# Optimization experiments

Measured on AMD Instinct MI355X. Metric: run time of the kernel, lower is better.

## Reference

```python
import jax, jax.numpy as jnp
import numpy as np

K = 7
TOWERS = 4
X_SIZE = 8
POS_SIZE = 3
NUM_GRAPHS = 128
NODES_PER_GRAPH = 512
N = NUM_GRAPHS * NODES_PER_GRAPH
EPS_STD = 1e-5  # PyG StdAggregation eps
BN_EPS = 1e-5
# degree histogram passed to PNAConv.__init__ -> avg log-degree used by scalers
_DEG_HIST = np.array([0, 0, 0, 0, 0, 100, 200, 700], dtype=np.float64)
_BINS = np.arange(_DEG_HIST.shape[0], dtype=np.float64)
AVG_DEG_LOG = float((np.log(_BINS + 1.0) * _DEG_HIST).sum() / _DEG_HIST.sum())


def knn_graph(pos, num_graphs, k):
    # batched kNN (loop=False): each node gets its k nearest neighbors within its graph
    Nn, D = pos.shape
    n = Nn // num_graphs
    p = pos.reshape(num_graphs, n, D)
    d2 = jnp.sum((p[:, :, None, :] - p[:, None, :, :]) ** 2, axis=-1)  # [B,n,n]
    d2 = d2 + jnp.eye(n, dtype=d2.dtype) * 1e10  # exclude self-loops
    _, idx = jax.lax.top_k(-d2, k)  # [B,n,k] local neighbor ids
    offs = (jnp.arange(num_graphs) * n)[:, None, None]
    return (idx + offs).reshape(Nn, k)  # global source ids per target node


def pna_conv(x, nbr, W_pre, b_pre, W_post, b_post, W_lin, b_lin):
    # PyG PNAConv, towers=4, pre_layers=1, post_layers=1, divide_input=False, edge_dim=None
    Nn, F = x.shape
    k = nbr.shape[1]
    x_j = x[nbr]                                              # gather sources [N,k,F]
    x_i = jnp.broadcast_to(x[:, None, :], (Nn, k, F))         # target features
    h = jnp.concatenate([x_i, x_j], axis=-1)                  # [N,k,2F]
    m = jnp.einsum('nke,tef->nktf', h, W_pre) + b_pre         # per-tower pre-MLP [N,k,T,F]
    mean = m.mean(axis=1)
    mn = m.min(axis=1)
    mx = m.max(axis=1)
    var = jnp.mean(m * m, axis=1) - mean * mean               # PyG VarAggregation
    std = jnp.sqrt(jax.nn.relu(var) + EPS_STD)
    agg = jnp.concatenate([mean, mn, mx, std], axis=-1)       # [N,T,4F]
    amp = jnp.log(k + 1.0) / AVG_DEG_LOG                      # deg == k for every node in a knn graph
    scaled = jnp.concatenate([agg, agg * amp, agg * (1.0 / amp)], axis=-1)  # identity/amp/atten [N,T,12F]
    out = jnp.concatenate([jnp.broadcast_to(x[:, None, :], (Nn, TOWERS, F)), scaled], axis=-1)  # [N,T,13F]
    out = jnp.einsum('ntg,tgf->ntf', out, W_post) + b_post    # per-tower post-MLP [N,T,F_out]
    out = out.reshape(Nn, -1)
    return out @ W_lin + b_lin                                # mixing Linear(out,out)


def batch_norm(x, g, b):
    # training-mode BatchNorm1d over the node dimension
    mu = x.mean(axis=0)
    var = x.var(axis=0)
    return g * (x - mu) * jax.lax.rsqrt(var + BN_EPS) + b


def forward(x, pos, W_pre1, b_pre1, W_post1, b_post1, W_lin1, b_lin1, bn1_g, bn1_b,
            W_pre2, b_pre2, W_post2, b_post2, W_lin2, b_lin2, bn2_g, bn2_b, num_graphs):
    nbr = knn_graph(pos, num_graphs, K)
    h = jax.nn.relu(batch_norm(pna_conv(x, nbr, W_pre1, b_pre1, W_post1, b_post1, W_lin1, b_lin1), bn1_g, bn1_b))
    h = jax.nn.relu(batch_norm(pna_conv(h, nbr, W_pre2, b_pre2, W_post2, b_post2, W_lin2, b_lin2), bn2_g, bn2_b))
    return h.reshape(num_graphs, -1, h.shape[-1]).mean(axis=1)  # global mean pool -> [B,128]


def _winit(key, shape):
    fan_in = shape[-2]
    return (jax.random.normal(key, shape, dtype=jnp.float32) / jnp.sqrt(jnp.float32(fan_in))).astype(jnp.float32)


def setup_inputs() -> dict:
    key = jax.random.key(0)
    ks = jax.random.split(key, 8)
    F1, F2 = X_SIZE, 64
    return {
        'x': jax.random.normal(ks[0], (N, X_SIZE), dtype=jnp.float32),
        'pos': jax.random.normal(ks[1], (N, POS_SIZE), dtype=jnp.float32),
        'W_pre1': _winit(ks[2], (TOWERS, 2 * F1, F1)),
        'b_pre1': jnp.zeros((TOWERS, F1), jnp.float32),
        'W_post1': _winit(ks[3], (TOWERS, 13 * F1, 64 // TOWERS)),
        'b_post1': jnp.zeros((TOWERS, 64 // TOWERS), jnp.float32),
        'W_lin1': _winit(ks[4], (64, 64)),
        'b_lin1': jnp.zeros((64,), jnp.float32),
        'bn1_g': jnp.ones((64,), jnp.float32),
        'bn1_b': jnp.zeros((64,), jnp.float32),
        'W_pre2': _winit(ks[5], (TOWERS, 2 * F2, F2)),
        'b_pre2': jnp.zeros((TOWERS, F2), jnp.float32),
        'W_post2': _winit(ks[6], (TOWERS, 13 * F2, 128 // TOWERS)),
        'b_post2': jnp.zeros((TOWERS, 128 // TOWERS), jnp.float32),
        'W_lin2': _winit(ks[7], (128, 128)),
        'b_lin2': jnp.zeros((128,), jnp.float32),
        'bn2_g': jnp.ones((128,), jnp.float32),
        'bn2_b': jnp.zeros((128,), jnp.float32),
        'num_graphs': NUM_GRAPHS,
    }


def reference(x, pos, W_pre1, b_pre1, W_post1, b_post1, W_lin1, b_lin1, bn1_g, bn1_b,
              W_pre2, b_pre2, W_post2, b_post2, W_lin2, b_lin2, bn2_g, bn2_b, num_graphs):
    return forward(x, pos, W_pre1, b_pre1, W_post1, b_post1, W_lin1, b_lin1, bn1_g, bn1_b,
                   W_pre2, b_pre2, W_post2, b_post2, W_lin2, b_lin2, bn2_g, bn2_b, num_graphs)
```

## Files before the change

kernel.cpp:

```cpp
#include <hip/hip_runtime.h>
#include <math.h>


#define NGRAPH 128
#define NPG    512
#define NN     (NGRAPH*NPG)
#define KNB    7

constexpr double AVG_DEG_LOG_D = 2.0239670479173344;
constexpr double LOG8_D        = 2.0794415416798357;

typedef _Float16 f16x8 __attribute__((ext_vector_type(8)));
typedef _Float16 h2    __attribute__((ext_vector_type(2)));
typedef float    f32x4 __attribute__((ext_vector_type(4)));

__device__ __forceinline__ unsigned short f2h(float x) {
    _Float16 h = (_Float16)x;
    return __builtin_bit_cast(unsigned short, h);
}

__global__ __launch_bounds__(256) void prep_kernel(
    const float* __restrict__ Wpost1, const float* __restrict__ Wpost2,
    const float* __restrict__ Wpre2,  const float* __restrict__ Wlin2,
    const float* __restrict__ Wlin1,  const float* __restrict__ bpost1,
    const float* __restrict__ blin1,
    const float* __restrict__ bpost2, const float* __restrict__ blin2,
    unsigned short* __restrict__ Wf1p, unsigned short* __restrict__ Wf1l,
    float* __restrict__ blin1_eff,
    unsigned short* __restrict__ Wfuv,
    unsigned short* __restrict__ Wfp, unsigned short* __restrict__ Wfl,
    float* __restrict__ blin_eff)
{
    const float AMP = (float)(LOG8_D / AVG_DEG_LOG_D);
    const float ATT = (float)(AVG_DEG_LOG_D / LOG8_D);
    for (int i = blockIdx.x*256 + threadIdx.x; i < 98496; i += gridDim.x*256) {
        if (i < 4096) {
            int t = i >> 10, kk = (i >> 9) & 1, lane = (i >> 3) & 63, j = i & 7;
            int k = kk*32 + ((lane >> 4) << 3) + j;
            int col = lane & 15;
            float val;
            if (k < 8)       val = Wpost1[(t*104 + k)*16 + col];
            else if (k < 40) {
                int g2 = k - 8;
                val = Wpost1[(t*104 +  8 + g2)*16 + col]
                    + AMP*Wpost1[(t*104 + 40 + g2)*16 + col]
                    + ATT*Wpost1[(t*104 + 72 + g2)*16 + col];
            } else val = 0.f;
            Wf1p[i] = f2h(val);
        } else if (i < 8192) {
            int jj = i - 4096;
            int kk = jj >> 11, tile = (jj >> 9) & 3, lane = (jj >> 3) & 63, j = jj & 7;
            int k = kk*32 + ((lane >> 4) << 3) + j;
            int col = tile*16 + (lane & 15);
            Wf1l[jj] = f2h(Wlin1[k*64 + col]);
        } else if (i < 8256) {
            int c = i - 8192;
            float s = blin1[c];
            for (int o = 0; o < 64; ++o) s += bpost1[o]*Wlin1[o*64 + c];
            blin1_eff[c] = s;
        } else if (i < 41024) {
            int jj = i - 8256;
            int kk = jj >> 14, ct = (jj >> 9) & 31, lane = (jj >> 3) & 63, jf = jj & 7;
            int k   = kk*32 + ((lane >> 4) << 3) + jf;
            int col = ct*16 + (lane & 15);
            float val;
            if (col < 256) { int t = col >> 6, f = col & 63; val = Wpre2[(t*128 +      k)*64 + f]; }
            else { int c2 = col - 256; int t = c2 >> 6, f = c2 & 63; val = Wpre2[(t*128 + 64 + k)*64 + f]; }
            Wfuv[jj] = f2h(val);
        } else if (i < 81984) {
            int jj = i - 41024;
            int t = jj / 10240, r = jj % 10240;
            int kk = r / 1024, r2 = r % 1024;
            int c = r2 >> 9, lane = (r2 >> 3) & 63, jf = r2 & 7;
            int G   = kk*32 + ((lane >> 4) << 3) + jf;
            int col = c*16 + (lane & 15);
            float val;
            if (G < 64) val = Wpost2[(t*832 + G)*32 + col];
            else {
                int g2 = G - 64;
                val = Wpost2[(t*832 +  64 + g2)*32 + col]
                    + AMP*Wpost2[(t*832 + 320 + g2)*32 + col]
                    + ATT*Wpost2[(t*832 + 576 + g2)*32 + col];
            }
            Wfp[jj] = f2h(val);
        } else if (i < 98368) {
            int jj = i - 81984;
            int kk = jj / 4096, r = jj % 4096;
            int tile = r >> 9, lane = (r >> 3) & 63, jf = r & 7;
            int k   = kk*32 + ((lane >> 4) << 3) + jf;
            int col = tile*16 + (lane & 15);
            Wfl[jj] = f2h(Wlin2[k*128 + col]);
        } else {
            int c = i - 98368;
            float s = blin2[c];
            for (int o = 0; o < 128; ++o) s += bpost2[o]*Wlin2[o*128 + c];
            blin_eff[c] = s;
        }
    }
}

__global__ __launch_bounds__(256) void knn_kernel(const float* __restrict__ pos, int* __restrict__ nbr)
{
    __shared__ float4 posS[NPG];
    const int g    = blockIdx.x >> 1;
    const int half = blockIdx.x & 1;
    const int gb   = g * NPG;
    for (int j = threadIdx.x; j < NPG; j += 256)
        posS[j] = make_float4(pos[(gb+j)*3+0], pos[(gb+j)*3+1], pos[(gb+j)*3+2], 0.f);
    __syncthreads();
    const int i = half*256 + threadIdx.x;
    const float4 pi = posS[i];
    float bd[KNB]; int bi[KNB];
#pragma unroll
    for (int e = 0; e < KNB; ++e) { bd[e] = 3.0e38f; bi[e] = -1; }
#pragma unroll 4
    for (int j = 0; j < NPG; ++j) {
        float4 pj = posS[j];
        float dx = pi.x - pj.x, dy = pi.y - pj.y, dz = pi.z - pj.z;
        float d2 = __fadd_rn(__fadd_rn(__fmul_rn(dx,dx), __fmul_rn(dy,dy)), __fmul_rn(dz,dz));
        if (j == i) d2 = __builtin_inff();
        bool cmp[KNB];
#pragma unroll
        for (int e = 0; e < KNB; ++e) cmp[e] = d2 < bd[e];
#pragma unroll
        for (int e = KNB-1; e >= 1; --e) {
            bd[e] = cmp[e-1] ? bd[e-1] : (cmp[e] ? d2 : bd[e]);
            bi[e] = cmp[e-1] ? bi[e-1] : (cmp[e] ? j  : bi[e]);
        }
        bd[0] = cmp[0] ? d2 : bd[0];
        bi[0] = cmp[0] ? j  : bi[0];
    }
#pragma unroll
    for (int e = 0; e < KNB; ++e) nbr[(gb+i)*KNB + e] = gb + bi[e];
}

__global__ __launch_bounds__(256) void a1_kernel(
    const float* __restrict__ x, const float* __restrict__ Wpre1, const float* __restrict__ bpre1,
    float* __restrict__ u1, float* __restrict__ v1)
{
    __shared__ float wS[512];
    __shared__ float bS[32];
    const int tid = threadIdx.x;
    wS[tid] = Wpre1[tid]; wS[tid+256] = Wpre1[tid+256];
    if (tid < 32) bS[tid] = bpre1[tid];
    __syncthreads();
    const int n  = blockIdx.x*8 + (tid>>5);
    const int tf = tid & 31;
    const int t = tf >> 3, f = tf & 7;
    float u = bS[tf], v = 0.f;
#pragma unroll
    for (int e = 0; e < 8; ++e) {
        float xv = x[n*8+e];
        u += xv * wS[(t*16 + e)*8 + f];
        v += xv * wS[(t*16 + 8 + e)*8 + f];
    }
    u1[n*32+tf] = u;
    v1[n*32+tf] = v;
}

__global__ __launch_bounds__(256) void b1_kernel(
    const float* __restrict__ x, const int* __restrict__ nbr,
    const float* __restrict__ u1, const float* __restrict__ v1,
    const unsigned short* __restrict__ Wf1p, const unsigned short* __restrict__ Wf1l,
    const float* __restrict__ blin1_eff,
    float* __restrict__ y1)
{
    __shared__ int nbrsS[112];
    __shared__ __align__(16) unsigned short actS[64*72];
    __shared__ __align__(16) unsigned short postS[16*72];
    const int tid  = threadIdx.x;
    const int base = blockIdx.x * 16;
    if (tid < 112) nbrsS[tid] = nbr[base*7 + tid];
    for (int i = tid; i < 384; i += 256) {
        int r = i / 6, gq = i - 6*r;
        *(ushort4*)&actS[r*72 + 40 + gq*4] = make_ushort4(0,0,0,0);
    }
#pragma unroll
    for (int it = 0; it < 2; ++it) {
        int i = tid + it*256;
        int n = i >> 5, r2 = i & 31, t = r2 >> 3, f = r2 & 7;
        actS[(n*4 + t)*72 + f] = f2h(x[(base+n)*8 + f]);
    }
    __syncthreads();
    {
        const int n = tid >> 4, cp = tid & 15;
        const int tf0 = cp*2, t = tf0 >> 3, f0 = tf0 & 7;
        float2 uu = *(const float2*)&u1[(base+n)*32 + tf0];
        float s0=0.f,s1=0.f,q0=0.f,q1=0.f;
        float mn0=3e38f,mn1=3e38f,mx0=-3e38f,mx1=-3e38f;
#pragma unroll
        for (int e = 0; e < 7; ++e) {
            float2 vv = *(const float2*)&v1[nbrsS[n*7+e]*32 + tf0];
            s0 += vv.x; q0 += vv.x*vv.x; mn0 = fminf(mn0, vv.x); mx0 = fmaxf(mx0, vv.x);
            s1 += vv.y; q1 += vv.y*vv.y; mn1 = fminf(mn1, vv.y); mx1 = fmaxf(mx1, vv.y);
        }
        float me0 = s0*(1.f/7.f), me1 = s1*(1.f/7.f);
        float sd0 = sqrtf(fmaxf(q0*(1.f/7.f) - me0*me0, 0.f) + 1e-5f);
        float sd1 = sqrtf(fmaxf(q1*(1.f/7.f) - me1*me1, 0.f) + 1e-5f);
        const int row = (n*4 + t)*72;
        ushort2 w_;
        w_.x = f2h(uu.x + me0); w_.y = f2h(uu.y + me1); *(ushort2*)&actS[row +  8 + f0] = w_;
        w_.x = f2h(uu.x + mn0); w_.y = f2h(uu.y + mn1); *(ushort2*)&actS[row + 16 + f0] = w_;
        w_.x = f2h(uu.x + mx0); w_.y = f2h(uu.y + mx1); *(ushort2*)&actS[row + 24 + f0] = w_;
        w_.x = f2h(sd0);        w_.y = f2h(sd1);        *(ushort2*)&actS[row + 32 + f0] = w_;
    }
    __syncthreads();
    const int l = tid & 63, w = tid >> 6;
    const int lr = l & 15, lk = l >> 4;
    f32x4 acc = {0.f,0.f,0.f,0.f};
    {
        const f16x8* WB = (const f16x8*)Wf1p;
#pragma unroll
        for (int kk = 0; kk < 2; ++kk) {
            f16x8 a = *(const f16x8*)&actS[(lr*4 + w)*72 + kk*32 + lk*8];
            f16x8 b = WB[(w*2 + kk)*64 + l];
            acc = __builtin_amdgcn_mfma_f32_16x16x32_f16(a, b, acc, 0, 0, 0);
        }
    }
#pragma unroll
    for (int j = 0; j < 4; ++j)
        postS[(lk*4 + j)*72 + w*16 + lr] = f2h(acc[j]);
    __syncthreads();
    f32x4 d = {0.f,0.f,0.f,0.f};
    {
        const f16x8* WB = (const f16x8*)Wf1l;
#pragma unroll
        for (int kk = 0; kk < 2; ++kk) {
            f16x8 a = *(const f16x8*)&postS[lr*72 + kk*32 + lk*8];
            f16x8 b = WB[(kk*4 + w)*64 + l];
            d = __builtin_amdgcn_mfma_f32_16x16x32_f16(a, b, d, 0, 0, 0);
        }
    }
    const float be = blin1_eff[w*16 + lr];
#pragma unroll
    for (int j = 0; j < 4; ++j)
        y1[(base + lk*4 + j)*64 + w*16 + lr] = d[j] + be;
}

template<int C>
__global__ __launch_bounds__(256) void bn_stats_kernel(
    const float* __restrict__ y, float* __restrict__ Ps, float* __restrict__ Pq)
{
    constexpr int IT     = (NN/1024)*(C/4)/256;
    constexpr int GROUPS = C/4;
    constexpr int REPS   = 256/GROUPS;
    const int tid = threadIdx.x;
    const float4* y4 = (const float4*)y + (size_t)blockIdx.x*256*IT;
    float4 s = make_float4(0.f,0.f,0.f,0.f), q = make_float4(0.f,0.f,0.f,0.f);
#pragma unroll
    for (int it = 0; it < IT; ++it) {
        float4 v = y4[it*256 + tid];
        s.x += v.x; s.y += v.y; s.z += v.z; s.w += v.w;
        q.x += v.x*v.x; q.y += v.y*v.y; q.z += v.z*v.z; q.w += v.w*v.w;
    }
    __shared__ float4 sS[256], qS[256];
    sS[tid] = s; qS[tid] = q;
    __syncthreads();
#pragma unroll
    for (int step = REPS/2; step >= 1; step >>= 1) {
        if (tid < step*GROUPS) {
            float4 s2 = sS[tid + step*GROUPS], q2 = qS[tid + step*GROUPS];
            float4 ss = sS[tid], qq = qS[tid];
            ss.x += s2.x; ss.y += s2.y; ss.z += s2.z; ss.w += s2.w;
            qq.x += q2.x; qq.y += q2.y; qq.z += q2.z; qq.w += q2.w;
            sS[tid] = ss; qS[tid] = qq;
        }
        __syncthreads();
    }
    if (tid < GROUPS) {
        ((float4*)&Ps[(size_t)blockIdx.x*C])[tid] = sS[tid];
        ((float4*)&Pq[(size_t)blockIdx.x*C])[tid] = qS[tid];
    }
}

template<int C>
__global__ __launch_bounds__(C) void finA_kernel(
    const float* __restrict__ Ps, const float* __restrict__ Pq,
    float* __restrict__ As, float* __restrict__ Aq)
{
    const int c = threadIdx.x, b = blockIdx.x;
    float s = 0.f, q = 0.f;
#pragma unroll
    for (int i = 0; i < 16; ++i) {
        s += Ps[(b*16 + i)*C + c];
        q += Pq[(b*16 + i)*C + c];
    }
    As[b*C + c] = s;
    Aq[b*C + c] = q;
}

template<int C>
__global__ __launch_bounds__(C) void fin_kernel(
    const float* __restrict__ As, const float* __restrict__ Aq,
    const float* __restrict__ g, const float* __restrict__ b,
    float* __restrict__ scO, float* __restrict__ shO)
{
    const int c = threadIdx.x;
    float s = 0.f, q = 0.f;
#pragma unroll 8
    for (int i = 0; i < 64; ++i) { s += As[i*C + c]; q += Aq[i*C + c]; }
    const float inv = 1.f/(float)NN;
    float mu  = s*inv;
    float var = q*inv - mu*mu;
    float sc  = g[c]*rsqrtf(var + 1e-5f);
    scO[c] = sc;
    shO[c] = b[c] - mu*sc;
}

__global__ __launch_bounds__(256) void a2_kernel(
    const float* __restrict__ y1raw, const float* __restrict__ sc1, const float* __restrict__ sh1,
    const unsigned short* __restrict__ Wfuv, const float* __restrict__ bpre2,
    unsigned short* __restrict__ uv2)
{
    __shared__ __align__(16) unsigned short a1S[64*72];
    __shared__ float biasS[256];
    const int tid  = threadIdx.x;
    const int base = blockIdx.x * 64;
    biasS[tid] = bpre2[tid];
#pragma unroll
    for (int it = 0; it < 4; ++it) {
        int i = tid + it*256;
        float4 vv = ((const float4*)y1raw)[blockIdx.x*1024 + i];
        int n = i >> 4, c0 = (i & 15)*4;
        float c_[4] = {vv.x, vv.y, vv.z, vv.w};
#pragma unroll
        for (int j = 0; j < 4; ++j) {
            int c = c0 + j;
            a1S[n*72 + c] = f2h(fmaxf(c_[j]*sc1[c] + sh1[c], 0.f));
        }
    }
    __syncthreads();
    const int l = tid & 63, w = tid >> 6;
    const int lr = l & 15, lk = l >> 4;
    const f16x8 a0  = *(const f16x8*)&a1S[(w*16 + lr)*72 +      lk*8];
    const f16x8 a1f = *(const f16x8*)&a1S[(w*16 + lr)*72 + 32 + lk*8];
    const f16x8* WB = (const f16x8*)Wfuv;
#pragma unroll 4
    for (int ct = 0; ct < 32; ++ct) {
        f32x4 acc = {0.f,0.f,0.f,0.f};
        f16x8 b0 = WB[ct*64 + l];
        f16x8 b1 = WB[(32 + ct)*64 + l];
        acc = __builtin_amdgcn_mfma_f32_16x16x32_f16(a0,  b0, acc, 0, 0, 0);
        acc = __builtin_amdgcn_mfma_f32_16x16x32_f16(a1f, b1, acc, 0, 0, 0);
        const int col = ct*16 + lr;
        const float bias = (ct < 16) ? biasS[col] : 0.f;
#pragma unroll
        for (int j = 0; j < 4; ++j)
            uv2[(base + w*16 + lk*4 + j)*512 + col] = f2h(acc[j] + bias);
    }
}

__global__ __launch_bounds__(256) void b2_kernel(
    const int* __restrict__ nbr, const float* __restrict__ y1raw,
    const float* __restrict__ sc1, const float* __restrict__ sh1,
    const unsigned short* __restrict__ uv2,
    const unsigned short* __restrict__ Wfp, const unsigned short* __restrict__ Wfl,
    const float* __restrict__ blin_eff,
    float* __restrict__ y2)
{
    __shared__ int nbrsS[112];
    __shared__ __align__(16) unsigned short a1S[16*72];
    __shared__ __align__(16) unsigned short aggS[64*264];
    __shared__ __align__(16) unsigned short postS[16*136];

    const int tid = threadIdx.x;
    const int ob   = blockIdx.x;
    const int xcd  = ob & 7, slot = ob >> 3;
    const int gph  = ((slot >> 5) << 3) + xcd;
    const int sub  = slot & 31;
    const int base = gph*NPG + sub*16;

    if (tid < 112) nbrsS[tid] = nbr[base*7 + tid];
    for (int i = tid; i < 1024; i += 256) {
        int c = i & 63, n = i >> 6;
        float a = fmaxf(y1raw[base*64 + i]*sc1[c] + sh1[c], 0.f);
        a1S[n*72 + c] = f2h(a);
    }
    __syncthreads();
    {
        const int ns = tid >> 6, cg = tid & 63;
        const int t = cg >> 4, f0 = (cg & 15) * 4;
        const h2 inv7 = { (_Float16)(1.f/7.f), (_Float16)(1.f/7.f) };
#pragma unroll
        for (int it = 0; it < 4; ++it) {
            const int ln = it*4 + ns;
            uint2 uu = *(const uint2*)&uv2[(size_t)(base+ln)*512 + cg*4];
            h2 u01 = __builtin_bit_cast(h2, uu.x);
            h2 u23 = __builtin_bit_cast(h2, uu.y);
            h2 z = { (_Float16)0.f, (_Float16)0.f };
            h2 s01 = z, s23 = z, q01 = z, q23 = z;
            h2 mn01 = { (_Float16)65504.f, (_Float16)65504.f }, mn23 = mn01;
            h2 mx01 = { (_Float16)-65504.f, (_Float16)-65504.f }, mx23 = mx01;
#pragma unroll
            for (int e = 0; e < 7; ++e) {
                uint2 vv = *(const uint2*)&uv2[(size_t)nbrsS[ln*7+e]*512 + 256 + cg*4];
                h2 v01 = __builtin_bit_cast(h2, vv.x);
                h2 v23 = __builtin_bit_cast(h2, vv.y);
                s01 += v01; s23 += v23;
                q01 += v01*v01; q23 += v23*v23;
                mn01 = __builtin_elementwise_min(mn01, v01);
                mn23 = __builtin_elementwise_min(mn23, v23);
                mx01 = __builtin_elementwise_max(mx01, v01);
                mx23 = __builtin_elementwise_max(mx23, v23);
            }
            h2 me01 = s01*inv7, me23 = s23*inv7;
            h2 om01 = u01 + me01, om23 = u23 + me23;
            h2 on01 = u01 + mn01, on23 = u23 + mn23;
            h2 ox01 = u01 + mx01, ox23 = u23 + mx23;
            float m0 = (float)me01[0], m1 = (float)me01[1];
            float m2 = (float)me23[0], m3 = (float)me23[1];
            float sd0 = sqrtf(fmaxf(fmaf((float)q01[0], 1.f/7.f, -m0*m0), 0.f) + 1e-5f);
            float sd1 = sqrtf(fmaxf(fmaf((float)q01[1], 1.f/7.f, -m1*m1), 0.f) + 1e-5f);
            float sd2 = sqrtf(fmaxf(fmaf((float)q23[0], 1.f/7.f, -m2*m2), 0.f) + 1e-5f);
            float sd3 = sqrtf(fmaxf(fmaf((float)q23[1], 1.f/7.f, -m3*m3), 0.f) + 1e-5f);
            h2 sd01 = { (_Float16)sd0, (_Float16)sd1 };
            h2 sd23 = { (_Float16)sd2, (_Float16)sd3 };
            const int ro = (t*16 + ln)*264 + f0;
            *(uint2*)&aggS[ro      ] = make_uint2(__builtin_bit_cast(unsigned, om01), __builtin_bit_cast(unsigned, om23));
            *(uint2*)&aggS[ro +  64] = make_uint2(__builtin_bit_cast(unsigned, on01), __builtin_bit_cast(unsigned, on23));
            *(uint2*)&aggS[ro + 128] = make_uint2(__builtin_bit_cast(unsigned, ox01), __builtin_bit_cast(unsigned, ox23));
            *(uint2*)&aggS[ro + 192] = make_uint2(__builtin_bit_cast(unsigned, sd01), __builtin_bit_cast(unsigned, sd23));
        }
    }
    __syncthreads();
    const int l = tid & 63, w = tid >> 6;
    const int lr = l & 15, lk = l >> 4;
    f32x4 acc0 = {0.f,0.f,0.f,0.f}, acc1 = {0.f,0.f,0.f,0.f};
    {
        const f16x8* WB = (const f16x8*)Wfp;
#pragma unroll
        for (int kk = 0; kk < 10; ++kk) {
            f16x8 a;
            if (kk < 2) a = *(const f16x8*)&a1S[lr*72 + kk*32 + lk*8];
            else        a = *(const f16x8*)&aggS[(w*16 + lr)*264 + (kk-2)*32 + lk*8];
            f16x8 b0 = WB[((w*10 + kk)*2 + 0)*64 + l];
            f16x8 b1 = WB[((w*10 + kk)*2 + 1)*64 + l];
            acc0 = __builtin_amdgcn_mfma_f32_16x16x32_f16(a, b0, acc0, 0, 0, 0);
            acc1 = __builtin_amdgcn_mfma_f32_16x16x32_f16(a, b1, acc1, 0, 0, 0);
        }
    }
#pragma unroll
    for (int j = 0; j < 4; ++j) {
        const int row = lk*4 + j;
        postS[row*136 + w*32 +      lr] = f2h(acc0[j]);
        postS[row*136 + w*32 + 16 + lr] = f2h(acc1[j]);
    }
    __syncthreads();
    f32x4 d0 = {0.f,0.f,0.f,0.f}, d1 = {0.f,0.f,0.f,0.f};
    {
        const f16x8* WB = (const f16x8*)Wfl;
#pragma unroll
        for (int kk = 0; kk < 4; ++kk) {
            f16x8 a = *(const f16x8*)&postS[lr*136 + kk*32 + lk*8];
            f16x8 b0 = WB[(kk*8 + 2*w + 0)*64 + l];
            f16x8 b1 = WB[(kk*8 + 2*w + 1)*64 + l];
            d0 = __builtin_amdgcn_mfma_f32_16x16x32_f16(a, b0, d0, 0, 0, 0);
            d1 = __builtin_amdgcn_mfma_f32_16x16x32_f16(a, b1, d1, 0, 0, 0);
        }
    }
    const float be0 = blin_eff[w*32 +      lr];
    const float be1 = blin_eff[w*32 + 16 + lr];
#pragma unroll
    for (int j = 0; j < 4; ++j) {
        const int row = lk*4 + j;
        y2[(base + row)*128 + w*32 +      lr] = d0[j] + be0;
        y2[(base + row)*128 + w*32 + 16 + lr] = d1[j] + be1;
    }
}

__global__ __launch_bounds__(128) void pool_part_kernel(
    const float* __restrict__ y2, const float* __restrict__ sc2, const float* __restrict__ sh2,
    float* __restrict__ Pp)
{
    const int c = threadIdx.x;
    const int b = blockIdx.x;
    const float sc = sc2[c];
    const float sh = sh2[c];
    float acc = 0.f;
    const size_t base = (size_t)b*64*128 + c;
#pragma unroll 4
    for (int i = 0; i < 64; ++i)
        acc += fmaxf(y2[base + (size_t)i*128]*sc + sh, 0.f);
    Pp[b*128 + c] = acc;
}

__global__ __launch_bounds__(128) void pool_fin_kernel(
    const float* __restrict__ Pp, float* __restrict__ out)
{
    const int c = threadIdx.x, g = blockIdx.x;
    float acc = 0.f;
#pragma unroll
    for (int i = 0; i < 8; ++i) acc += Pp[(g*8 + i)*128 + c];
    out[g*128 + c] = acc * (1.f/(float)NPG);
}

extern "C" void kernel_launch(void* const* d_in, const int* in_sizes, int n_in,
                              void* d_out, int out_size, void* d_ws, size_t ws_size,
                              hipStream_t stream)
{
    const float* x      = (const float*)d_in[0];
    const float* pos    = (const float*)d_in[1];
    const float* Wpre1  = (const float*)d_in[2];
    const float* bpre1  = (const float*)d_in[3];
    const float* Wpost1 = (const float*)d_in[4];
    const float* bpost1 = (const float*)d_in[5];
    const float* Wlin1  = (const float*)d_in[6];
    const float* blin1  = (const float*)d_in[7];
    const float* bn1g   = (const float*)d_in[8];
    const float* bn1b   = (const float*)d_in[9];
    const float* Wpre2  = (const float*)d_in[10];
    const float* bpre2  = (const float*)d_in[11];
    const float* Wpost2 = (const float*)d_in[12];
    const float* bpost2 = (const float*)d_in[13];
    const float* Wlin2  = (const float*)d_in[14];
    const float* blin2  = (const float*)d_in[15];
    const float* bn2g   = (const float*)d_in[16];
    const float* bn2b   = (const float*)d_in[17];
    float* out = (float*)d_out;

    char* ws = (char*)d_ws;
    size_t off = 0;
    auto alloc = [&](size_t bytes) { void* p = ws + off; off += (bytes + 255) & ~(size_t)255; return p; };
    int*   nbr   = (int*)  alloc((size_t)NN*7*4);
    float* u1    = (float*)alloc((size_t)NN*32*4);
    float* v1    = (float*)alloc((size_t)NN*32*4);
    float* y1    = (float*)alloc((size_t)NN*64*4);
    unsigned short* uv2 = (unsigned short*)alloc((size_t)NN*512*2);
    float* y2    = (float*)alloc((size_t)NN*128*4);
    unsigned short* Wf1p = (unsigned short*)alloc(4096*2);
    unsigned short* Wf1l = (unsigned short*)alloc(4096*2);
    float* blin1_eff = (float*)alloc(64*4);
    unsigned short* Wfuv = (unsigned short*)alloc(32768*2);
    unsigned short* Wfp  = (unsigned short*)alloc(40960*2);
    unsigned short* Wfl  = (unsigned short*)alloc(16384*2);
    float* blin_eff = (float*)alloc(128*4);
    float* P1s   = (float*)alloc(1024*64*4);
    float* P1q   = (float*)alloc(1024*64*4);
    float* A1s   = (float*)alloc(64*64*4);
    float* A1q   = (float*)alloc(64*64*4);
    float* sc1   = (float*)alloc(64*4);
    float* sh1   = (float*)alloc(64*4);
    float* P2s   = (float*)alloc(1024*128*4);
    float* P2q   = (float*)alloc(1024*128*4);
    float* A2s   = (float*)alloc(64*128*4);
    float* A2q   = (float*)alloc(64*128*4);
    float* sc2   = (float*)alloc(128*4);
    float* sh2   = (float*)alloc(128*4);
    float* Pp    = (float*)alloc(1024*128*4);

    prep_kernel<<<128, 256, 0, stream>>>(Wpost1, Wpost2, Wpre2, Wlin2, Wlin1, bpost1, blin1,
                                         bpost2, blin2,
                                         Wf1p, Wf1l, blin1_eff, Wfuv, Wfp, Wfl, blin_eff);
    knn_kernel<<<NGRAPH*2, 256, 0, stream>>>(pos, nbr);
    a1_kernel<<<NN/8, 256, 0, stream>>>(x, Wpre1, bpre1, u1, v1);
    b1_kernel<<<NN/16, 256, 0, stream>>>(x, nbr, u1, v1, Wf1p, Wf1l, blin1_eff, y1);
    bn_stats_kernel<64><<<1024, 256, 0, stream>>>(y1, P1s, P1q);
    finA_kernel<64><<<64, 64, 0, stream>>>(P1s, P1q, A1s, A1q);
    fin_kernel<64><<<1, 64, 0, stream>>>(A1s, A1q, bn1g, bn1b, sc1, sh1);
    a2_kernel<<<NN/64, 256, 0, stream>>>(y1, sc1, sh1, Wfuv, bpre2, uv2);
    b2_kernel<<<NN/16, 256, 0, stream>>>(nbr, y1, sc1, sh1, uv2, Wfp, Wfl, blin_eff, y2);
    bn_stats_kernel<128><<<1024, 256, 0, stream>>>(y2, P2s, P2q);
    finA_kernel<128><<<64, 128, 0, stream>>>(P2s, P2q, A2s, A2q);
    fin_kernel<128><<<1, 128, 0, stream>>>(A2s, A2q, bn2g, bn2b, sc2, sh2);
    pool_part_kernel<<<1024, 128, 0, stream>>>(y2, sc2, sh2, Pp);
    pool_fin_kernel<<<NGRAPH, 128, 0, stream>>>(Pp, out);
}
```

Baseline: 181.1 us.

## Split kNN search into candidate-chunk partial top-k plus merge kernel

The kNN kernel is split along the candidate dimension. Each block now scans a 128-candidate quarter of a graph and writes a partial top-7 of (distance, index) pairs, and a second kernel merges the four partial lists per node. This raises the grid from 256 to 1024 blocks so the GPU is better occupied during the serial 512-candidate scan. The cost is an extra launch and a round trip of partial results through global memory. Ties are resolved the same way as before because chunks are merged in ascending index order.

```diff
diff --git a/kernel.cpp b/kernel.cpp
--- a/kernel.cpp
+++ b/kernel.cpp
@@ -99,39 +99,74 @@
     }
 }
 
-__global__ __launch_bounds__(256) void knn_kernel(const float* __restrict__ pos, int* __restrict__ nbr)
-{
-    __shared__ float4 posS[NPG];
-    const int g    = blockIdx.x >> 1;
-    const int half = blockIdx.x & 1;
-    const int gb   = g * NPG;
-    for (int j = threadIdx.x; j < NPG; j += 256)
-        posS[j] = make_float4(pos[(gb+j)*3+0], pos[(gb+j)*3+1], pos[(gb+j)*3+2], 0.f);
-    __syncthreads();
-    const int i = half*256 + threadIdx.x;
-    const float4 pi = posS[i];
+__global__ __launch_bounds__(256) void knn_part_kernel(const float* __restrict__ pos, float2* __restrict__ part)
+{
+    __shared__ float4 cposS[128];
+    const int b = blockIdx.x;
+    const int g = b >> 3, h = (b >> 2) & 1, q = b & 3;
+    const int gb = g * NPG;
+    const int cbase = q * 128;
+    if (threadIdx.x < 128) {
+        int j = cbase + threadIdx.x;
+        cposS[threadIdx.x] = make_float4(pos[(gb+j)*3+0], pos[(gb+j)*3+1], pos[(gb+j)*3+2], 0.f);
+    }
+    __syncthreads();
+    const int i = h*256 + threadIdx.x;
+    const float px = pos[(gb+i)*3+0], py = pos[(gb+i)*3+1], pz = pos[(gb+i)*3+2];
     float bd[KNB]; int bi[KNB];
 #pragma unroll
     for (int e = 0; e < KNB; ++e) { bd[e] = 3.0e38f; bi[e] = -1; }
 #pragma unroll 4
-    for (int j = 0; j < NPG; ++j) {
-        float4 pj = posS[j];
-        float dx = pi.x - pj.x, dy = pi.y - pj.y, dz = pi.z - pj.z;
+    for (int j = 0; j < 128; ++j) {
+        float4 pj = cposS[j];
+        float dx = px - pj.x, dy = py - pj.y, dz = pz - pj.z;
         float d2 = __fadd_rn(__fadd_rn(__fmul_rn(dx,dx), __fmul_rn(dy,dy)), __fmul_rn(dz,dz));
-        if (j == i) d2 = __builtin_inff();
+        if (cbase + j == i) d2 = __builtin_inff();
         bool cmp[KNB];
 #pragma unroll
         for (int e = 0; e < KNB; ++e) cmp[e] = d2 < bd[e];
 #pragma unroll
         for (int e = KNB-1; e >= 1; --e) {
             bd[e] = cmp[e-1] ? bd[e-1] : (cmp[e] ? d2 : bd[e]);
-            bi[e] = cmp[e-1] ? bi[e-1] : (cmp[e] ? j  : bi[e]);
+            bi[e] = cmp[e-1] ? bi[e-1] : (cmp[e] ? cbase + j : bi[e]);
         }
         bd[0] = cmp[0] ? d2 : bd[0];
-        bi[0] = cmp[0] ? j  : bi[0];
-    }
-#pragma unroll
-    for (int e = 0; e < KNB; ++e) nbr[(gb+i)*KNB + e] = gb + bi[e];
+        bi[0] = cmp[0] ? cbase + j : bi[0];
+    }
+    float2* dst = &part[((size_t)(g*NPG + i)*4 + q)*KNB];
+#pragma unroll
+    for (int e = 0; e < KNB; ++e) dst[e] = make_float2(bd[e], __int_as_float(bi[e]));
+}
+
+__global__ __launch_bounds__(256) void knn_merge_kernel(const float2* __restrict__ part, int* __restrict__ nbr)
+{
+    const int n = blockIdx.x*256 + threadIdx.x;
+    const float4* p4 = (const float4*)&part[(size_t)n*28];
+    float bd[KNB]; int bi[KNB];
+#pragma unroll
+    for (int e = 0; e < KNB; ++e) { bd[e] = 3.0e38f; bi[e] = -1; }
+#pragma unroll
+    for (int m4 = 0; m4 < 14; ++m4) {
+        float4 pr = p4[m4];
+#pragma unroll
+        for (int half = 0; half < 2; ++half) {
+            float d2  = half ? pr.z : pr.x;
+            int   idx = __float_as_int(half ? pr.w : pr.y);
+            bool cmp[KNB];
+#pragma unroll
+            for (int e = 0; e < KNB; ++e) cmp[e] = d2 < bd[e];
+#pragma unroll
+            for (int e = KNB-1; e >= 1; --e) {
+                bd[e] = cmp[e-1] ? bd[e-1] : (cmp[e] ? d2 : bd[e]);
+                bi[e] = cmp[e-1] ? bi[e-1] : (cmp[e] ? idx : bi[e]);
+            }
+            bd[0] = cmp[0] ? d2 : bd[0];
+            bi[0] = cmp[0] ? idx : bi[0];
+        }
+    }
+    const int gb = n & ~(NPG-1);
+#pragma unroll
+    for (int e = 0; e < KNB; ++e) nbr[n*KNB + e] = gb + bi[e];
 }
 
 __global__ __launch_bounds__(256) void a1_kernel(
@@ -521,7 +556,8 @@
     char* ws = (char*)d_ws;
     size_t off = 0;
     auto alloc = [&](size_t bytes) { void* p = ws + off; off += (bytes + 255) & ~(size_t)255; return p; };
-    int*   nbr   = (int*)  alloc((size_t)NN*7*4);
+    int*    nbr  = (int*)   alloc((size_t)NN*7*4);
+    float2* part = (float2*)alloc((size_t)NN*28*8);
     float* u1    = (float*)alloc((size_t)NN*32*4);
     float* v1    = (float*)alloc((size_t)NN*32*4);
     float* y1    = (float*)alloc((size_t)NN*64*4);
@@ -551,7 +587,8 @@
     prep_kernel<<<128, 256, 0, stream>>>(Wpost1, Wpost2, Wpre2, Wlin2, Wlin1, bpost1, blin1,
                                          bpost2, blin2,
                                          Wf1p, Wf1l, blin1_eff, Wfuv, Wfp, Wfl, blin_eff);
-    knn_kernel<<<NGRAPH*2, 256, 0, stream>>>(pos, nbr);
+    knn_part_kernel<<<NGRAPH*8, 256, 0, stream>>>(pos, part);
+    knn_merge_kernel<<<NN/256, 256, 0, stream>>>(part, nbr);
     a1_kernel<<<NN/8, 256, 0, stream>>>(x, Wpre1, bpre1, u1, v1);
     b1_kernel<<<NN/16, 256, 0, stream>>>(x, nbr, u1, v1, Wf1p, Wf1l, blin1_eff, y1);
     bn_stats_kernel<64><<<1024, 256, 0, stream>>>(y1, P1s, P1q);
```

After: 175.7 us. -3.0%, faster.
